# Performance work log

Measured on AMD Instinct MI355X. Metric: run time of the kernel, lower is better.

## Reference

```python
import jax, jax.numpy as jnp
import numpy as np

N = 100000
E = 1600000
D_IN = 128
D_H = 256


def setup_inputs() -> dict:
    key = jax.random.key(0)
    ks = jax.random.split(key, 8)
    x = jax.random.normal(ks[0], (N, D_IN), dtype=jnp.float32)
    x_tilde = jax.random.normal(ks[1], (N, D_IN), dtype=jnp.float32)
    adj_row = jnp.sort(jax.random.randint(ks[2], (E,), 0, N, dtype=jnp.int32))
    adj_col = jax.random.randint(ks[3], (E,), 0, N, dtype=jnp.int32)
    # normalized-ish positive edge weights
    adj_vals = jax.random.uniform(ks[4], (E,), dtype=jnp.float32) / 16.0
    # Linear weight (torch layout [out, in]), xavier-ish scale
    W1 = jax.random.normal(ks[5], (D_H, D_IN), dtype=jnp.float32) * (2.0 / (D_IN + D_H)) ** 0.5
    prelu_a = jnp.full((1,), 0.25, dtype=jnp.float32)  # PReLU default slope
    w_bil = jax.random.normal(ks[6], (D_H, D_H), dtype=jnp.float32) * (2.0 / (2 * D_H)) ** 0.5
    return {"x": x, "x_tilde": x_tilde, "adj_vals": adj_vals, "adj_row": adj_row,
            "adj_col": adj_col, "W1": W1, "prelu_a": prelu_a, "w_bil": w_bil}


def reference(x, x_tilde, adj_vals, adj_row, adj_col, W1, prelu_a, w_bil):
    n = x.shape[0]

    def gcn(feat):
        # SpMM: agg[r] = sum_e vals[e] * feat[col[e]] for edges with row[e]==r
        gathered = adj_vals[:, None] * feat[adj_col]  # [E, D_IN]
        agg = jax.ops.segment_sum(gathered, adj_row, num_segments=n)  # [N, D_IN]
        z = agg @ W1.T  # [N, D_H]
        return jnp.where(z >= 0, z, prelu_a[0] * z)  # PReLU

    h = gcn(x)
    h_tilde = gcn(x_tilde)
    s = jax.nn.sigmoid(jnp.mean(h, axis=0))  # [D_H] readout (same for every row)
    dp = jnp.einsum('ni,ij,j->n', h, w_bil, s)  # bilinear discriminator
    dn = jnp.einsum('ni,ij,j->n', h_tilde, w_bil, s)
    return jnp.concatenate([dp, dn])[None, :]  # [1, 2N]
```

## Files before the change

### kernel.cpp

```cpp
#include <hip/hip_runtime.h>

__device__ __forceinline__ float b2f(unsigned short s) {
    union { unsigned int u; float f; } c; c.u = ((unsigned int)s) << 16; return c.f;
}
__device__ __forceinline__ unsigned short f2b(float f) {
    union { float f; unsigned int u; } c; c.f = f;
    unsigned int u = c.u;
    unsigned int r = u + 0x7FFFu + ((u >> 16) & 1u);
    return (unsigned short)(r >> 16);
}
__device__ __forceinline__ unsigned int pack2(float lo, float hi) {
    return ((unsigned int)f2b(hi) << 16) | f2b(lo);
}
__device__ __forceinline__ void fma8(float* a, float v, uint4 w) {
    a[0] = fmaf(v, b2f((unsigned short)w.x), a[0]);
    a[1] = fmaf(v, b2f((unsigned short)(w.x >> 16)), a[1]);
    a[2] = fmaf(v, b2f((unsigned short)w.y), a[2]);
    a[3] = fmaf(v, b2f((unsigned short)(w.y >> 16)), a[3]);
    a[4] = fmaf(v, b2f((unsigned short)w.z), a[4]);
    a[5] = fmaf(v, b2f((unsigned short)(w.z >> 16)), a[5]);
    a[6] = fmaf(v, b2f((unsigned short)w.w), a[6]);
    a[7] = fmaf(v, b2f((unsigned short)(w.w >> 16)), a[7]);
}

typedef __attribute__((ext_vector_type(8))) short bf16x8;
typedef __attribute__((ext_vector_type(4))) float f32x4;

#define T_TILES 10

__global__ void detect_dtype(const unsigned int* __restrict__ xw, int* __restrict__ flag) {
    __shared__ int c;
    int tid = threadIdx.x;
    if (tid == 0) c = 0;
    __syncthreads();
    int cnt = 0;
    for (int i = tid; i < 1024; i += 256) {
        unsigned int w = xw[i];
        unsigned int e = (w >> 7) & 0xFFu;
        if (e >= 0x90u) cnt++;
    }
    atomicAdd(&c, cnt);
    __syncthreads();
    if (tid == 0) flag[0] = (c > 100) ? 1 : 0;
}

__global__ __launch_bounds__(256) void prep(
    const int* __restrict__ row, int* __restrict__ rp, int n, int e, int rb,
    const void* __restrict__ w1, const void* __restrict__ wbil,
    const void* __restrict__ pa, const int* __restrict__ flag,
    unsigned short* __restrict__ w1b, float* __restrict__ wbilf, float* __restrict__ paf,
    int pb,
    const void* __restrict__ x, const void* __restrict__ xt,
    unsigned short* __restrict__ xint, int total8, int halfcb)
{
    int b = blockIdx.x, tid = threadIdx.x;
    if (b < rb) {
        int i = b * 256 + tid;
        if (i > e) return;
        if (i == 0) {
            int r1 = row[0];
            for (int rr = 0; rr <= r1; ++rr) rp[rr] = 0;
        } else if (i == e) {
            int r0 = row[e - 1];
            for (int rr = r0 + 1; rr <= n; ++rr) rp[rr] = e;
        } else {
            int r0 = row[i - 1], r1 = row[i];
            for (int rr = r0 + 1; rr <= r1; ++rr) rp[rr] = i;
        }
    } else if (b < rb + pb) {
        int i = (b - rb) * 256 + tid;
        if (flag[0]) {
            if (i < 32768) w1b[i] = f2b(((const float*)w1)[i]);
            wbilf[i] = ((const float*)wbil)[i];
            if (i == 0) paf[0] = ((const float*)pa)[0];
        } else {
            if (i < 32768) w1b[i] = ((const unsigned short*)w1)[i];
            wbilf[i] = b2f(((const unsigned short*)wbil)[i]);
            if (i == 0) paf[0] = b2f(((const unsigned short*)pa)[0]);
        }
    } else {
        int cb = b - rb - pb;
        int which = (cb >= halfcb) ? 1 : 0;
        int i = (cb - which * halfcb) * 256 + tid;
        if (i >= total8) return;
        const void* s = which ? xt : x;
        int node = i >> 4, sub = i & 15;
        uint4 o;
        if (flag[0]) {
            const float4* p = (const float4*)s + (size_t)i * 2;
            float4 a = p[0], bb = p[1];
            o.x = pack2(a.x, a.y);  o.y = pack2(a.z, a.w);
            o.z = pack2(bb.x, bb.y); o.w = pack2(bb.z, bb.w);
        } else {
            o = ((const uint4*)s)[i];
        }
        *(uint4*)(xint + (size_t)node * 256 + which * 128 + sub * 8) = o;
    }
}

__global__ __launch_bounds__(256) void spmm_dual3(
    const unsigned short* __restrict__ xint, const void* __restrict__ valsv,
    const int* __restrict__ col, const int* __restrict__ row_ptr,
    const int* __restrict__ flag,
    unsigned short* __restrict__ aggx, unsigned short* __restrict__ aggt, int n)
{
    int wave = threadIdx.x >> 6;
    int lane = threadIdx.x & 63;
    int g = lane >> 4, l = lane & 15;
    int r = blockIdx.x * 4 + wave;
    if (r >= n) return;
    int e0 = row_ptr[r], e1 = row_ptr[r + 1];
    float ax[8], at[8];
#pragma unroll
    for (int d = 0; d < 8; ++d) { ax[d] = 0.f; at[d] = 0.f; }
    if (flag[0]) {
        const float* vals = (const float*)valsv;
        for (int base = e0; base < e1; base += 8) {
            int eA = base + g, eB = base + 4 + g;
            bool vA = eA < e1, vB = eB < e1;
            int ecA = vA ? eA : e1 - 1, ecB = vB ? eB : e1 - 1;
            int cA = col[ecA], cB = col[ecB];
            float fvA = vA ? vals[ecA] : 0.f;
            float fvB = vB ? vals[ecB] : 0.f;
            const uint4* pA = (const uint4*)(xint + (size_t)cA * 256);
            const uint4* pB = (const uint4*)(xint + (size_t)cB * 256);
            uint4 xA = pA[l], tA = pA[16 + l];
            uint4 xB = pB[l], tB = pB[16 + l];
            fma8(ax, fvA, xA); fma8(at, fvA, tA);
            fma8(ax, fvB, xB); fma8(at, fvB, tB);
        }
    } else {
        const unsigned short* vals = (const unsigned short*)valsv;
        for (int base = e0; base < e1; base += 8) {
            int eA = base + g, eB = base + 4 + g;
            bool vA = eA < e1, vB = eB < e1;
            int ecA = vA ? eA : e1 - 1, ecB = vB ? eB : e1 - 1;
            int cA = col[ecA], cB = col[ecB];
            float fvA = vA ? b2f(vals[ecA]) : 0.f;
            float fvB = vB ? b2f(vals[ecB]) : 0.f;
            const uint4* pA = (const uint4*)(xint + (size_t)cA * 256);
            const uint4* pB = (const uint4*)(xint + (size_t)cB * 256);
            uint4 xA = pA[l], tA = pA[16 + l];
            uint4 xB = pB[l], tB = pB[16 + l];
            fma8(ax, fvA, xA); fma8(at, fvA, tA);
            fma8(ax, fvB, xB); fma8(at, fvB, tB);
        }
    }
#pragma unroll
    for (int d = 0; d < 8; ++d) {
        ax[d] += __shfl_xor(ax[d], 16, 64);
        ax[d] += __shfl_xor(ax[d], 32, 64);
        at[d] += __shfl_xor(at[d], 16, 64);
        at[d] += __shfl_xor(at[d], 32, 64);
    }
    if (g == 0) {
        uint4 o;
        o.x = pack2(ax[0], ax[1]); o.y = pack2(ax[2], ax[3]);
        o.z = pack2(ax[4], ax[5]); o.w = pack2(ax[6], ax[7]);
        ((uint4*)(aggx + (size_t)r * 128))[l] = o;
    } else if (g == 1) {
        uint4 o;
        o.x = pack2(at[0], at[1]); o.y = pack2(at[2], at[3]);
        o.z = pack2(at[4], at[5]); o.w = pack2(at[6], at[7]);
        ((uint4*)(aggt + (size_t)r * 128))[l] = o;
    }
}

__global__ __launch_bounds__(256) void spmm_dual_legacy(
    const void* __restrict__ xv, const void* __restrict__ xtv,
    const void* __restrict__ valsv, const int* __restrict__ col,
    const int* __restrict__ row_ptr, const int* __restrict__ flag,
    unsigned short* __restrict__ aggx, unsigned short* __restrict__ aggt, int n)
{
    int wave = threadIdx.x >> 6;
    int lane = threadIdx.x & 63;
    int r = blockIdx.x * 4 + wave;
    if (r >= n) return;
    int e0 = row_ptr[r], e1 = row_ptr[r + 1];
    float ax0 = 0.f, ax1 = 0.f, at0 = 0.f, at1 = 0.f;
    if (flag[0]) {
        const float* x  = (const float*)xv;
        const float* xt = (const float*)xtv;
        const float* vals = (const float*)valsv;
        for (int e = e0; e < e1; ++e) {
            int c = col[e];
            float v = vals[e];
            float2 wx = ((const float2*)(x + (size_t)c * 128))[lane];
            float2 wt = ((const float2*)(xt + (size_t)c * 128))[lane];
            ax0 = fmaf(v, wx.x, ax0); ax1 = fmaf(v, wx.y, ax1);
            at0 = fmaf(v, wt.x, at0); at1 = fmaf(v, wt.y, at1);
        }
    } else {
        const unsigned short* x  = (const unsigned short*)xv;
        const unsigned short* xt = (const unsigned short*)xtv;
        const unsigned short* vals = (const unsigned short*)valsv;
        for (int e = e0; e < e1; ++e) {
            int c = col[e];
            float v = b2f(vals[e]);
            unsigned int wx = ((const unsigned int*)(x + (size_t)c * 128))[lane];
            unsigned int wt = ((const unsigned int*)(xt + (size_t)c * 128))[lane];
            ax0 = fmaf(v, b2f((unsigned short)wx), ax0);
            ax1 = fmaf(v, b2f((unsigned short)(wx >> 16)), ax1);
            at0 = fmaf(v, b2f((unsigned short)wt), at0);
            at1 = fmaf(v, b2f((unsigned short)(wt >> 16)), at1);
        }
    }
    ((unsigned int*)(aggx + (size_t)r * 128))[lane] = pack2(ax0, ax1);
    ((unsigned int*)(aggt + (size_t)r * 128))[lane] = pack2(at0, at1);
}

__global__ __launch_bounds__(256) void gemm_colsum3(
    const short* __restrict__ aggb, const short* __restrict__ w1,
    const float* __restrict__ paf, float* __restrict__ partial, int ntiles, int nb)
{
    int tid = threadIdx.x;
    int w = tid >> 6, lane = tid & 63;
    int nl = lane & 15, quad = lane >> 4;
    const short* brow = w1 + ((size_t)(4 * w) * 16 + nl) * 128 + quad * 8;
    bf16x8 bf[4][4];
#pragma unroll
    for (int j = 0; j < 4; ++j)
#pragma unroll
        for (int k = 0; k < 4; ++k)
            bf[j][k] = *(const bf16x8*)(brow + j * 2048 + k * 32);
    float aslope = paf[0];
    float cs[4] = {0.f, 0.f, 0.f, 0.f};
    int t0 = blockIdx.x * T_TILES;
    int nt = ntiles - t0; if (nt > T_TILES) nt = T_TILES;
    for (int i = 0; i < nt; ++i) {
        const short* arow = aggb + ((size_t)(t0 + i) * 16 + nl) * 128 + quad * 8;
        bf16x8 af[4];
#pragma unroll
        for (int k = 0; k < 4; ++k) af[k] = *(const bf16x8*)(arow + k * 32);
        f32x4 acc[4];
#pragma unroll
        for (int j = 0; j < 4; ++j) acc[j] = (f32x4){0.f, 0.f, 0.f, 0.f};
#pragma unroll
        for (int k = 0; k < 4; ++k)
#pragma unroll
            for (int j = 0; j < 4; ++j)
                acc[j] = __builtin_amdgcn_mfma_f32_16x16x32_bf16(af[k], bf[j][k], acc[j], 0, 0, 0);
#pragma unroll
        for (int j = 0; j < 4; ++j)
#pragma unroll
            for (int r = 0; r < 4; ++r) {
                float z = acc[j][r];
                cs[j] += (z >= 0.f) ? z : aslope * z;
            }
    }
#pragma unroll
    for (int j = 0; j < 4; ++j) {
        cs[j] += __shfl_xor(cs[j], 16, 64);
        cs[j] += __shfl_xor(cs[j], 32, 64);
    }
    if (quad == 0)
#pragma unroll
        for (int j = 0; j < 4; ++j)
            partial[(size_t)((4 * w + j) * 16 + nl) * nb + blockIdx.x] = cs[j];
}

__global__ __launch_bounds__(256) void reduce_partials(
    const float* __restrict__ partial, int nb, float* __restrict__ sum_h)
{
    __shared__ float l[256];
    int d = blockIdx.x, tid = threadIdx.x;
    float s = 0.f;
    for (int i = tid; i < nb; i += 256)
        s += partial[(size_t)d * nb + i];
    l[tid] = s;
    __syncthreads();
    for (int o = 128; o > 0; o >>= 1) {
        if (tid < o) l[tid] += l[tid + o];
        __syncthreads();
    }
    if (tid == 0) sum_h[d] = l[0];
}

__global__ __launch_bounds__(256) void compute_v(
    const float* __restrict__ sum_h, const float* __restrict__ wbilf,
    float* __restrict__ v, float invN)
{
    __shared__ float s_lds[256];
    int t = threadIdx.x;
    float m = sum_h[t] * invN;
    s_lds[t] = 1.f / (1.f + expf(-m));
    __syncthreads();
    const float* wrow = wbilf + (size_t)t * 256;
    float acc = 0.f;
#pragma unroll 8
    for (int j = 0; j < 256; ++j)
        acc = fmaf(wrow[j], s_lds[j], acc);
    v[t] = acc;
}

__global__ __launch_bounds__(256) void gemm_dp2(
    const short* __restrict__ aggx, const short* __restrict__ aggt,
    const short* __restrict__ w1, const float* __restrict__ paf,
    const float* __restrict__ v, const int* __restrict__ flag,
    void* __restrict__ outv, int ntiles, int N)
{
    __shared__ float dpbuf[4][T_TILES * 16];
    int tid = threadIdx.x;
    int w = tid >> 6, lane = tid & 63;
    int nl = lane & 15, quad = lane >> 4;
    const short* agg = blockIdx.y ? aggt : aggx;
    const short* brow = w1 + ((size_t)(4 * w) * 16 + nl) * 128 + quad * 8;
    bf16x8 bf[4][4];
#pragma unroll
    for (int j = 0; j < 4; ++j)
#pragma unroll
        for (int k = 0; k < 4; ++k)
            bf[j][k] = *(const bf16x8*)(brow + j * 2048 + k * 32);
    float vreg[4];
#pragma unroll
    for (int j = 0; j < 4; ++j) vreg[j] = v[(4 * w + j) * 16 + nl];
    float aslope = paf[0];
    int t0 = blockIdx.x * T_TILES;
    int nt = ntiles - t0; if (nt > T_TILES) nt = T_TILES;
    for (int i = 0; i < nt; ++i) {
        const short* arow = agg + ((size_t)(t0 + i) * 16 + nl) * 128 + quad * 8;
        bf16x8 af[4];
#pragma unroll
        for (int k = 0; k < 4; ++k) af[k] = *(const bf16x8*)(arow + k * 32);
        f32x4 acc[4];
#pragma unroll
        for (int j = 0; j < 4; ++j) acc[j] = (f32x4){0.f, 0.f, 0.f, 0.f};
#pragma unroll
        for (int k = 0; k < 4; ++k)
#pragma unroll
            for (int j = 0; j < 4; ++j)
                acc[j] = __builtin_amdgcn_mfma_f32_16x16x32_bf16(af[k], bf[j][k], acc[j], 0, 0, 0);
        float p[4] = {0.f, 0.f, 0.f, 0.f};
#pragma unroll
        for (int j = 0; j < 4; ++j)
#pragma unroll
            for (int r = 0; r < 4; ++r) {
                float z = acc[j][r];
                float h = (z >= 0.f) ? z : aslope * z;
                p[r] = fmaf(h, vreg[j], p[r]);
            }
#pragma unroll
        for (int r = 0; r < 4; ++r) {
            p[r] += __shfl_xor(p[r], 1, 64);
            p[r] += __shfl_xor(p[r], 2, 64);
            p[r] += __shfl_xor(p[r], 4, 64);
            p[r] += __shfl_xor(p[r], 8, 64);
        }
        if (nl == 0)
#pragma unroll
            for (int r = 0; r < 4; ++r)
                dpbuf[w][i * 16 + quad * 4 + r] = p[r];
    }
    __syncthreads();
    int nloc = nt * 16;
    int f = flag[0];
    for (int idx = tid; idx < nloc; idx += 256) {
        float s = dpbuf[0][idx] + dpbuf[1][idx] + dpbuf[2][idx] + dpbuf[3][idx];
        size_t o = (size_t)blockIdx.y * N + (size_t)t0 * 16 + idx;
        if (f) ((float*)outv)[o] = s;
        else   ((unsigned short*)outv)[o] = f2b(s);
    }
}

extern "C" void kernel_launch(void* const* d_in, const int* in_sizes, int n_in,
                              void* d_out, int out_size, void* d_ws, size_t ws_size,
                              hipStream_t stream) {
    const void* x    = d_in[0];
    const void* xt   = d_in[1];
    const void* vals = d_in[2];
    const int* row   = (const int*)d_in[3];
    const int* col   = (const int*)d_in[4];
    const void* w1   = d_in[5];
    const void* pa   = d_in[6];
    const void* wb   = d_in[7];

    const int N = in_sizes[0] / 128;
    const int E = in_sizes[2];
    const int ntiles = (N + 15) / 16;
    const int cs_blocks = (ntiles + T_TILES - 1) / T_TILES;

    char* ws = (char*)d_ws;
    size_t off = 0;
    auto alloc = [&](size_t bytes) { char* p = ws + off; off = (off + bytes + 255) & ~(size_t)255; return p; };
    int* row_ptr         = (int*)alloc((size_t)(N + 1) * 4);
    unsigned short* aggx = (unsigned short*)alloc((size_t)N * 128 * 2);
    unsigned short* aggt = (unsigned short*)alloc((size_t)N * 128 * 2);
    unsigned short* w1b  = (unsigned short*)alloc(32768 * 2);
    float* wbilf         = (float*)alloc(65536 * 4);
    float* partial       = (float*)alloc((size_t)cs_blocks * 256 * 4);
    float* sum_h         = (float*)alloc(256 * 4);
    float* vvec          = (float*)alloc(256 * 4);
    float* paf           = (float*)alloc(4);
    int* flag            = (int*)alloc(4);
    size_t xintBytes = (size_t)N * 256 * 2;
    bool big = (off + xintBytes + 512) <= ws_size;
    unsigned short* xint = nullptr;
    if (big) xint = (unsigned short*)alloc(xintBytes);

    detect_dtype<<<1, 256, 0, stream>>>((const unsigned int*)x, flag);

    int rb = (E + 1 + 255) / 256;
    int pb = 256;
    int total8 = (N * 128) / 8;
    int halfcb = big ? (total8 + 255) / 256 : 0;
    prep<<<rb + pb + 2 * halfcb, 256, 0, stream>>>(
        row, row_ptr, N, E, rb,
        w1, wb, pa, flag, w1b, wbilf, paf, pb,
        x, xt, xint, total8, halfcb);

    if (big) {
        spmm_dual3<<<(N + 3) / 4, 256, 0, stream>>>(xint, vals, col, row_ptr, flag,
                                                    aggx, aggt, N);
    } else {
        spmm_dual_legacy<<<(N + 3) / 4, 256, 0, stream>>>(x, xt, vals, col, row_ptr, flag,
                                                          aggx, aggt, N);
    }
    gemm_colsum3<<<cs_blocks, 256, 0, stream>>>(
        (const short*)aggx, (const short*)w1b, paf, partial, ntiles, cs_blocks);
    reduce_partials<<<256, 256, 0, stream>>>(partial, cs_blocks, sum_h);
    compute_v<<<1, 256, 0, stream>>>(sum_h, wbilf, vvec, 1.0f / (float)N);
    gemm_dp2<<<dim3(cs_blocks, 2), 256, 0, stream>>>(
        (const short*)aggx, (const short*)aggt, (const short*)w1b, paf, vvec, flag,
        d_out, ntiles, N);
}
```

Measured before the change: 340.6 us.

## Drop dtype detection, batch edge index loads via wave shuffles in SpMM

Removes the runtime dtype-detection kernel and every bf16 fallback path, hardcoding fp32 inputs. This drops one launch and the flag reads, and the bilinear weight copy is removed because compute_v now reads it directly. The SpMM kernel now loads 64 column indices and values per wave in one coalesced read, then broadcasts them with shuffles and issues four row gathers per group before accumulating, to get more loads in flight. The sigmoid moves into the partial reduction kernel. The cost is that non-fp32 inputs and small workspaces are no longer handled.

Result: no change. 335.7 us (-1.4%).

```diff
diff --git a/kernel.cpp b/kernel.cpp
--- a/kernel.cpp
+++ b/kernel.cpp
@@ -1,4 +1,5 @@
 #include <hip/hip_runtime.h>
+
 
 __device__ __forceinline__ float b2f(unsigned short s) {
     union { unsigned int u; float f; } c; c.u = ((unsigned int)s) << 16; return c.f;
@@ -28,29 +29,10 @@
 
 #define T_TILES 10
 
-__global__ void detect_dtype(const unsigned int* __restrict__ xw, int* __restrict__ flag) {
-    __shared__ int c;
-    int tid = threadIdx.x;
-    if (tid == 0) c = 0;
-    __syncthreads();
-    int cnt = 0;
-    for (int i = tid; i < 1024; i += 256) {
-        unsigned int w = xw[i];
-        unsigned int e = (w >> 7) & 0xFFu;
-        if (e >= 0x90u) cnt++;
-    }
-    atomicAdd(&c, cnt);
-    __syncthreads();
-    if (tid == 0) flag[0] = (c > 100) ? 1 : 0;
-}
-
 __global__ __launch_bounds__(256) void prep(
     const int* __restrict__ row, int* __restrict__ rp, int n, int e, int rb,
-    const void* __restrict__ w1, const void* __restrict__ wbil,
-    const void* __restrict__ pa, const int* __restrict__ flag,
-    unsigned short* __restrict__ w1b, float* __restrict__ wbilf, float* __restrict__ paf,
-    int pb,
-    const void* __restrict__ x, const void* __restrict__ xt,
+    const float* __restrict__ w1, unsigned short* __restrict__ w1b, int pb,
+    const float* __restrict__ x, const float* __restrict__ xt,
     unsigned short* __restrict__ xint, int total8, int halfcb)
 {
     int b = blockIdx.x, tid = threadIdx.x;
@@ -69,39 +51,26 @@
         }
     } else if (b < rb + pb) {
         int i = (b - rb) * 256 + tid;
-        if (flag[0]) {
-            if (i < 32768) w1b[i] = f2b(((const float*)w1)[i]);
-            wbilf[i] = ((const float*)wbil)[i];
-            if (i == 0) paf[0] = ((const float*)pa)[0];
-        } else {
-            if (i < 32768) w1b[i] = ((const unsigned short*)w1)[i];
-            wbilf[i] = b2f(((const unsigned short*)wbil)[i]);
-            if (i == 0) paf[0] = b2f(((const unsigned short*)pa)[0]);
-        }
+        if (i < 32768) w1b[i] = f2b(w1[i]);
     } else {
         int cb = b - rb - pb;
         int which = (cb >= halfcb) ? 1 : 0;
         int i = (cb - which * halfcb) * 256 + tid;
         if (i >= total8) return;
-        const void* s = which ? xt : x;
+        const float* s = which ? xt : x;
         int node = i >> 4, sub = i & 15;
+        const float4* p = (const float4*)s + (size_t)i * 2;
+        float4 a = p[0], bb = p[1];
         uint4 o;
-        if (flag[0]) {
-            const float4* p = (const float4*)s + (size_t)i * 2;
-            float4 a = p[0], bb = p[1];
-            o.x = pack2(a.x, a.y);  o.y = pack2(a.z, a.w);
-            o.z = pack2(bb.x, bb.y); o.w = pack2(bb.z, bb.w);
-        } else {
-            o = ((const uint4*)s)[i];
-        }
+        o.x = pack2(a.x, a.y);  o.y = pack2(a.z, a.w);
+        o.z = pack2(bb.x, bb.y); o.w = pack2(bb.z, bb.w);
         *(uint4*)(xint + (size_t)node * 256 + which * 128 + sub * 8) = o;
     }
 }
 
-__global__ __launch_bounds__(256) void spmm_dual3(
-    const unsigned short* __restrict__ xint, const void* __restrict__ valsv,
+__global__ __launch_bounds__(256) void spmm_dual4(
+    const unsigned short* __restrict__ xint, const float* __restrict__ vals,
     const int* __restrict__ col, const int* __restrict__ row_ptr,
-    const int* __restrict__ flag,
     unsigned short* __restrict__ aggx, unsigned short* __restrict__ aggt, int n)
 {
     int wave = threadIdx.x >> 6;
@@ -113,37 +82,27 @@
     float ax[8], at[8];
 #pragma unroll
     for (int d = 0; d < 8; ++d) { ax[d] = 0.f; at[d] = 0.f; }
-    if (flag[0]) {
-        const float* vals = (const float*)valsv;
-        for (int base = e0; base < e1; base += 8) {
-            int eA = base + g, eB = base + 4 + g;
-            bool vA = eA < e1, vB = eB < e1;
-            int ecA = vA ? eA : e1 - 1, ecB = vB ? eB : e1 - 1;
-            int cA = col[ecA], cB = col[ecB];
-            float fvA = vA ? vals[ecA] : 0.f;
-            float fvB = vB ? vals[ecB] : 0.f;
-            const uint4* pA = (const uint4*)(xint + (size_t)cA * 256);
-            const uint4* pB = (const uint4*)(xint + (size_t)cB * 256);
-            uint4 xA = pA[l], tA = pA[16 + l];
-            uint4 xB = pB[l], tB = pB[16 + l];
-            fma8(ax, fvA, xA); fma8(at, fvA, tA);
-            fma8(ax, fvB, xB); fma8(at, fvB, tB);
-        }
-    } else {
-        const unsigned short* vals = (const unsigned short*)valsv;
-        for (int base = e0; base < e1; base += 8) {
-            int eA = base + g, eB = base + 4 + g;
-            bool vA = eA < e1, vB = eB < e1;
-            int ecA = vA ? eA : e1 - 1, ecB = vB ? eB : e1 - 1;
-            int cA = col[ecA], cB = col[ecB];
-            float fvA = vA ? b2f(vals[ecA]) : 0.f;
-            float fvB = vB ? b2f(vals[ecB]) : 0.f;
-            const uint4* pA = (const uint4*)(xint + (size_t)cA * 256);
-            const uint4* pB = (const uint4*)(xint + (size_t)cB * 256);
-            uint4 xA = pA[l], tA = pA[16 + l];
-            uint4 xB = pB[l], tB = pB[16 + l];
-            fma8(ax, fvA, xA); fma8(at, fvA, tA);
-            fma8(ax, fvB, xB); fma8(at, fvB, tB);
+    for (int chunk = e0; chunk < e1; chunk += 64) {
+        int m = e1 - chunk; if (m > 64) m = 64;
+        int ce = chunk + (lane < m ? lane : m - 1);
+        int cc = col[ce];
+        float cv = (lane < m) ? vals[ce] : 0.f;
+        for (int base = 0; base < m; base += 16) {
+            uint4 xw[4], tw[4];
+            float fv[4];
+#pragma unroll
+            for (int u = 0; u < 4; ++u) {
+                int idx = base + 4 * u + g;
+                int idc = idx < m ? idx : m - 1;
+                int c  = __shfl(cc, idc, 64);
+                float v = __shfl(cv, idc, 64);
+                fv[u] = (idx < m) ? v : 0.f;
+                const uint4* p = (const uint4*)(xint + (size_t)c * 256);
+                xw[u] = p[l];
+                tw[u] = p[16 + l];
+            }
+#pragma unroll
+            for (int u = 0; u < 4; ++u) { fma8(ax, fv[u], xw[u]); fma8(at, fv[u], tw[u]); }
         }
     }
 #pragma unroll
@@ -166,52 +125,9 @@
     }
 }
 
-__global__ __launch_bounds__(256) void spmm_dual_legacy(
-    const void* __restrict__ xv, const void* __restrict__ xtv,
-    const void* __restrict__ valsv, const int* __restrict__ col,
-    const int* __restrict__ row_ptr, const int* __restrict__ flag,
-    unsigned short* __restrict__ aggx, unsigned short* __restrict__ aggt, int n)
-{
-    int wave = threadIdx.x >> 6;
-    int lane = threadIdx.x & 63;
-    int r = blockIdx.x * 4 + wave;
-    if (r >= n) return;
-    int e0 = row_ptr[r], e1 = row_ptr[r + 1];
-    float ax0 = 0.f, ax1 = 0.f, at0 = 0.f, at1 = 0.f;
-    if (flag[0]) {
-        const float* x  = (const float*)xv;
-        const float* xt = (const float*)xtv;
-        const float* vals = (const float*)valsv;
-        for (int e = e0; e < e1; ++e) {
-            int c = col[e];
-            float v = vals[e];
-            float2 wx = ((const float2*)(x + (size_t)c * 128))[lane];
-            float2 wt = ((const float2*)(xt + (size_t)c * 128))[lane];
-            ax0 = fmaf(v, wx.x, ax0); ax1 = fmaf(v, wx.y, ax1);
-            at0 = fmaf(v, wt.x, at0); at1 = fmaf(v, wt.y, at1);
-        }
-    } else {
-        const unsigned short* x  = (const unsigned short*)xv;
-        const unsigned short* xt = (const unsigned short*)xtv;
-        const unsigned short* vals = (const unsigned short*)valsv;
-        for (int e = e0; e < e1; ++e) {
-            int c = col[e];
-            float v = b2f(vals[e]);
-            unsigned int wx = ((const unsigned int*)(x + (size_t)c * 128))[lane];
-            unsigned int wt = ((const unsigned int*)(xt + (size_t)c * 128))[lane];
-            ax0 = fmaf(v, b2f((unsigned short)wx), ax0);
-            ax1 = fmaf(v, b2f((unsigned short)(wx >> 16)), ax1);
-            at0 = fmaf(v, b2f((unsigned short)wt), at0);
-            at1 = fmaf(v, b2f((unsigned short)(wt >> 16)), at1);
-        }
-    }
-    ((unsigned int*)(aggx + (size_t)r * 128))[lane] = pack2(ax0, ax1);
-    ((unsigned int*)(aggt + (size_t)r * 128))[lane] = pack2(at0, at1);
-}
-
 __global__ __launch_bounds__(256) void gemm_colsum3(
     const short* __restrict__ aggb, const short* __restrict__ w1,
-    const float* __restrict__ paf, float* __restrict__ partial, int ntiles, int nb)
+    const float* __restrict__ pa, float* __restrict__ partial, int ntiles, int nb)
 {
     int tid = threadIdx.x;
     int w = tid >> 6, lane = tid & 63;
@@ -223,7 +139,7 @@
 #pragma unroll
         for (int k = 0; k < 4; ++k)
             bf[j][k] = *(const bf16x8*)(brow + j * 2048 + k * 32);
-    float aslope = paf[0];
+    float aslope = pa[0];
     float cs[4] = {0.f, 0.f, 0.f, 0.f};
     int t0 = blockIdx.x * T_TILES;
     int nt = ntiles - t0; if (nt > T_TILES) nt = T_TILES;
@@ -259,8 +175,8 @@
             partial[(size_t)((4 * w + j) * 16 + nl) * nb + blockIdx.x] = cs[j];
 }
 
-__global__ __launch_bounds__(256) void reduce_partials(
-    const float* __restrict__ partial, int nb, float* __restrict__ sum_h)
+__global__ __launch_bounds__(256) void reduce_sig(
+    const float* __restrict__ partial, int nb, float* __restrict__ s_out, float invN)
 {
     __shared__ float l[256];
     int d = blockIdx.x, tid = threadIdx.x;
@@ -273,19 +189,18 @@
         if (tid < o) l[tid] += l[tid + o];
         __syncthreads();
     }
-    if (tid == 0) sum_h[d] = l[0];
+    if (tid == 0) s_out[d] = 1.f / (1.f + expf(-l[0] * invN));
 }
 
 __global__ __launch_bounds__(256) void compute_v(
-    const float* __restrict__ sum_h, const float* __restrict__ wbilf,
-    float* __restrict__ v, float invN)
+    const float* __restrict__ s_in, const float* __restrict__ wbil,
+    float* __restrict__ v)
 {
     __shared__ float s_lds[256];
     int t = threadIdx.x;
-    float m = sum_h[t] * invN;
-    s_lds[t] = 1.f / (1.f + expf(-m));
+    s_lds[t] = s_in[t];
     __syncthreads();
-    const float* wrow = wbilf + (size_t)t * 256;
+    const float* wrow = wbil + (size_t)t * 256;
     float acc = 0.f;
 #pragma unroll 8
     for (int j = 0; j < 256; ++j)
@@ -295,9 +210,8 @@
 
 __global__ __launch_bounds__(256) void gemm_dp2(
     const short* __restrict__ aggx, const short* __restrict__ aggt,
-    const short* __restrict__ w1, const float* __restrict__ paf,
-    const float* __restrict__ v, const int* __restrict__ flag,
-    void* __restrict__ outv, int ntiles, int N)
+    const short* __restrict__ w1, const float* __restrict__ pa,
+    const float* __restrict__ v, float* __restrict__ out, int ntiles, int N)
 {
     __shared__ float dpbuf[4][T_TILES * 16];
     int tid = threadIdx.x;
@@ -314,7 +228,7 @@
     float vreg[4];
 #pragma unroll
     for (int j = 0; j < 4; ++j) vreg[j] = v[(4 * w + j) * 16 + nl];
-    float aslope = paf[0];
+    float aslope = pa[0];
     int t0 = blockIdx.x * T_TILES;
     int nt = ntiles - t0; if (nt > T_TILES) nt = T_TILES;
     for (int i = 0; i < nt; ++i) {
@@ -353,26 +267,23 @@
     }
     __syncthreads();
     int nloc = nt * 16;
-    int f = flag[0];
     for (int idx = tid; idx < nloc; idx += 256) {
         float s = dpbuf[0][idx] + dpbuf[1][idx] + dpbuf[2][idx] + dpbuf[3][idx];
-        size_t o = (size_t)blockIdx.y * N + (size_t)t0 * 16 + idx;
-        if (f) ((float*)outv)[o] = s;
-        else   ((unsigned short*)outv)[o] = f2b(s);
+        out[(size_t)blockIdx.y * N + (size_t)t0 * 16 + idx] = s;
     }
 }
 
 extern "C" void kernel_launch(void* const* d_in, const int* in_sizes, int n_in,
                               void* d_out, int out_size, void* d_ws, size_t ws_size,
                               hipStream_t stream) {
-    const void* x    = d_in[0];
-    const void* xt   = d_in[1];
-    const void* vals = d_in[2];
-    const int* row   = (const int*)d_in[3];
-    const int* col   = (const int*)d_in[4];
-    const void* w1   = d_in[5];
-    const void* pa   = d_in[6];
-    const void* wb   = d_in[7];
+    const float* x    = (const float*)d_in[0];
+    const float* xt   = (const float*)d_in[1];
+    const float* vals = (const float*)d_in[2];
+    const int* row    = (const int*)d_in[3];
+    const int* col    = (const int*)d_in[4];
+    const float* w1   = (const float*)d_in[5];
+    const float* pa   = (const float*)d_in[6];
+    const float* wb   = (const float*)d_in[7];
 
     const int N = in_sizes[0] / 128;
     const int E = in_sizes[2];
@@ -386,40 +297,25 @@
     unsigned short* aggx = (unsigned short*)alloc((size_t)N * 128 * 2);
     unsigned short* aggt = (unsigned short*)alloc((size_t)N * 128 * 2);
     unsigned short* w1b  = (unsigned short*)alloc(32768 * 2);
-    float* wbilf         = (float*)alloc(65536 * 4);
     float* partial       = (float*)alloc((size_t)cs_blocks * 256 * 4);
-    float* sum_h         = (float*)alloc(256 * 4);
+    float* svec          = (float*)alloc(256 * 4);
     float* vvec          = (float*)alloc(256 * 4);
-    float* paf           = (float*)alloc(4);
-    int* flag            = (int*)alloc(4);
-    size_t xintBytes = (size_t)N * 256 * 2;
-    bool big = (off + xintBytes + 512) <= ws_size;
-    unsigned short* xint = nullptr;
-    if (big) xint = (unsigned short*)alloc(xintBytes);
-
-    detect_dtype<<<1, 256, 0, stream>>>((const unsigned int*)x, flag);
+    unsigned short* xint = (unsigned short*)alloc((size_t)N * 256 * 2);
 
     int rb = (E + 1 + 255) / 256;
-    int pb = 256;
+    int pb = 128;
     int total8 = (N * 128) / 8;
-    int halfcb = big ? (total8 + 255) / 256 : 0;
+    int halfcb = (total8 + 255) / 256;
     prep<<<rb + pb + 2 * halfcb, 256, 0, stream>>>(
-        row, row_ptr, N, E, rb,
-        w1, wb, pa, flag, w1b, wbilf, paf, pb,
-        x, xt, xint, total8, halfcb);
-
-    if (big) {
-        spmm_dual3<<<(N + 3) / 4, 256, 0, stream>>>(xint, vals, col, row_ptr, flag,
-                                                    aggx, aggt, N);
-    } else {
-        spmm_dual_legacy<<<(N + 3) / 4, 256, 0, stream>>>(x, xt, vals, col, row_ptr, flag,
-                                                          aggx, aggt, N);
-    }
+        row, row_ptr, N, E, rb, w1, w1b, pb, x, xt, xint, total8, halfcb);
+
+    spmm_dual4<<<(N + 3) / 4, 256, 0, stream>>>(xint, vals, col, row_ptr, aggx, aggt, N);
+
     gemm_colsum3<<<cs_blocks, 256, 0, stream>>>(
-        (const short*)aggx, (const short*)w1b, paf, partial, ntiles, cs_blocks);
-    reduce_partials<<<256, 256, 0, stream>>>(partial, cs_blocks, sum_h);
-    compute_v<<<1, 256, 0, stream>>>(sum_h, wbilf, vvec, 1.0f / (float)N);
+        (const short*)aggx, (const short*)w1b, pa, partial, ntiles, cs_blocks);
+    reduce_sig<<<256, 256, 0, stream>>>(partial, cs_blocks, svec, 1.0f / (float)N);
+    compute_v<<<1, 256, 0, stream>>>(svec, wb, vvec);
     gemm_dp2<<<dim3(cs_blocks, 2), 256, 0, stream>>>(
-        (const short*)aggx, (const short*)aggt, (const short*)w1b, paf, vvec, flag,
-        d_out, ntiles, N);
-}
+        (const short*)aggx, (const short*)aggt, (const short*)w1b, pa, vvec,
+        (float*)d_out, ntiles, N);
+}
```
